# Performance work log

Measured on AMD Instinct MI355X. Metric: run time of the kernel, lower is better.

## Reference

```python
import jax, jax.numpy as jnp
import numpy as np

N = 4096
C = 8192
D = 64
MARGIN = 0.1
ALPHA = 32.0


def setup_inputs() -> dict:
    key = jax.random.key(0)
    k1, k2, k3, k4 = jax.random.split(key, 4)
    embeddings = jax.random.normal(k1, (N, D), dtype=jnp.float32)
    labels = jax.random.randint(k2, (N,), 0, C)
    # kaiming_normal_(mode='fan_out') on a (C, D) tensor -> std = sqrt(2/C)
    mean_proxies = jax.random.normal(k3, (C, D), dtype=jnp.float32) * np.sqrt(2.0 / C)
    log_variance_proxies = jax.random.normal(k4, (C, D), dtype=jnp.float32) * np.sqrt(2.0 / C)
    return {
        "embeddings": embeddings,
        "labels": labels,
        "mean_proxies": mean_proxies,
        "log_variance_proxies": log_variance_proxies,
    }


def _mls_scores(e, mu, logvar):
    """score[i,j] = -0.5 * sum_d[(e_id - mu_jd)^2 * exp(-logvar_jd) + logvar_jd].
    Expanded into GEMMs to avoid materializing the (N, C, D) broadcast tensor."""
    inv_var = jnp.exp(-logvar)                                  # (C, D)
    e2_term = (e * e) @ inv_var.T                               # (N, C)
    cross = e @ (mu * inv_var).T                                # (N, C)
    const = jnp.sum(mu * mu * inv_var + logvar, axis=1)         # (C,)
    return -0.5 * (e2_term - 2.0 * cross + const[None, :])      # (N, C)


def reference(embeddings, labels, mean_proxies, log_variance_proxies):
    score_mat = _mls_scores(embeddings, mean_proxies, log_variance_proxies)  # (N, C)
    pos_mask = jax.nn.one_hot(labels, C, dtype=score_mat.dtype)              # (N, C)

    pos_e = -ALPHA * (score_mat - MARGIN)
    neg_e = ALPHA * (score_mat + MARGIN)
    m = jnp.max(pos_e)  # NOTE: original code uses max(pos_exp) for BOTH terms
    pos_exp = jnp.exp(pos_e - m)
    neg_exp = jnp.exp(neg_e - m)

    counts = jnp.sum(pos_mask, axis=0)                   # (C,)
    num_valid = jnp.sum(counts != 0).astype(score_mat.dtype)

    pos_sim_sum = jnp.sum(jnp.where(pos_mask == 1, pos_exp, 0.0), axis=0)  # (C,)
    neg_sim_sum = jnp.sum(jnp.where(pos_mask == 0, neg_exp, 0.0), axis=0)  # (C,)

    pos_term = jnp.sum(jnp.log1p(pos_sim_sum) + m) / num_valid
    neg_term = jnp.sum(jnp.log1p(neg_sim_sum) + m) / C
    return pos_term + neg_term
```

## Files before the change

kernel.cpp:

```cpp
#include <hip/hip_runtime.h>
#include <hip/hip_bf16.h>
#include <math.h>


#define N_EMB 4096
#define C_CLS 8192
#define D_DIM 64
#define K_DIM 128
#define NCB 4

#define S2_F    23.083120654223414f
#define B2_F     4.616624130844683f
#define NEGC2_F  9.233248261689366f
#define LN2_F    0.6931471805599453f

typedef __attribute__((ext_vector_type(8))) __bf16 bf16x8;
typedef __attribute__((ext_vector_type(4))) __bf16 bf16x4;
typedef __attribute__((ext_vector_type(16))) float f32x16;
typedef __attribute__((ext_vector_type(4))) int i32x4;

__device__ __forceinline__ void async_ld16(void* lds, const void* g) {
  __builtin_amdgcn_global_load_lds(
      (__attribute__((address_space(1))) void*)g,
      (__attribute__((address_space(3))) void*)lds, 16, 0, 0);
}

__device__ __forceinline__ float fexp2(float x) {
  float r;
  asm("v_exp_f32 %0, %1" : "=v"(r) : "v"(x));
  return r;
}

__global__ void k_prep(const float* __restrict__ emb,
                       const float* __restrict__ mp,
                       const float* __restrict__ lvp,
                       __bf16* __restrict__ wsA,
                       __bf16* __restrict__ wsB,
                       float* __restrict__ constv) {
  const int wave = (int)((blockIdx.x * blockDim.x + threadIdx.x) >> 6);
  const int lane = threadIdx.x & 63;
  const int sub = lane >> 4, q = lane & 15;
  const int row = wave * 4 + sub;
  if (row < N_EMB) {
    float4 e4 = *(const float4*)&emb[row * D_DIM + q * 4];
    bf16x4 sq = {(__bf16)(e4.x * e4.x), (__bf16)(e4.y * e4.y),
                 (__bf16)(e4.z * e4.z), (__bf16)(e4.w * e4.w)};
    bf16x4 ev = {(__bf16)e4.x, (__bf16)e4.y, (__bf16)e4.z, (__bf16)e4.w};
    *(bf16x4*)&wsA[row * K_DIM + q * 4] = sq;
    *(bf16x4*)&wsA[row * K_DIM + D_DIM + q * 4] = ev;
  } else {
    const int j = row - N_EMB;
    float4 mu4 = *(const float4*)&mp[j * D_DIM + q * 4];
    float4 lv4 = *(const float4*)&lvp[j * D_DIM + q * 4];
    float iv0 = __expf(-lv4.x), iv1 = __expf(-lv4.y);
    float iv2 = __expf(-lv4.z), iv3 = __expf(-lv4.w);
    bf16x4 ivv = {(__bf16)iv0, (__bf16)iv1, (__bf16)iv2, (__bf16)iv3};
    bf16x4 mv = {(__bf16)(-2.0f * mu4.x * iv0), (__bf16)(-2.0f * mu4.y * iv1),
                 (__bf16)(-2.0f * mu4.z * iv2), (__bf16)(-2.0f * mu4.w * iv3)};
    *(bf16x4*)&wsB[j * K_DIM + q * 4] = ivv;
    *(bf16x4*)&wsB[j * K_DIM + D_DIM + q * 4] = mv;
    float t = fmaf(mu4.x * mu4.x, iv0, lv4.x)
            + fmaf(mu4.y * mu4.y, iv1, lv4.y)
            + fmaf(mu4.z * mu4.z, iv2, lv4.z)
            + fmaf(mu4.w * mu4.w, iv3, lv4.w);
    #pragma unroll
    for (int s = 8; s >= 1; s >>= 1) t += __shfl_xor(t, s);
    if (q == 0) constv[j] = t;
  }
}

__global__ __launch_bounds__(256, 2) void k_main(
    const __bf16* __restrict__ wsA, const __bf16* __restrict__ wsB,
    const float* __restrict__ constv, const int* __restrict__ labels,
    float* __restrict__ wsM, float* __restrict__ wsP, float* __restrict__ wsN) {
  __shared__ __align__(16) char As[32768];
  __shared__ __align__(16) char Bs[32768];
  __shared__ float colred[2][128][3];

  const int tid = threadIdx.x;
  const int rb  = blockIdx.x & 31;
  const int cbg = blockIdx.x >> 5;

  const char* Ag = (const char*)(wsA + (size_t)rb * 128 * K_DIM);
  const char* Bgb = (const char*)(wsB + (size_t)(cbg * NCB) * 128 * K_DIM);
  #pragma unroll
  for (int it = 0; it < 8; ++it) {
    int L = it * 256 + tid;
    int r = L >> 4, cs = L & 15;
    int goff = r * 256 + ((cs ^ (r & 15)) << 4);
    async_ld16(As + L * 16, Ag + goff);
  }
  #pragma unroll
  for (int it = 0; it < 8; ++it) {
    int L = it * 256 + tid;
    int r = L >> 4, cs = L & 15;
    int goff = r * 256 + ((cs ^ (r & 15)) << 4);
    async_ld16(Bs + L * 16, Bgb + goff);
  }

  const int wv = tid >> 6, lane = tid & 63;
  const int wr = wv >> 1, wc = wv & 1;
  const int l31 = lane & 31, kg = lane >> 5;
  const int l15 = lane & 15;

  i32x4 labv[2][4];
  #pragma unroll
  for (int mi = 0; mi < 2; ++mi)
    #pragma unroll
    for (int g = 0; g < 4; ++g)
      labv[mi][g] = *(const i32x4*)&labels[rb * 128 + wr * 64 + mi * 32 +
                                           4 * kg + 8 * g];
  float cvv[NCB][2];
  #pragma unroll
  for (int cbi = 0; cbi < NCB; ++cbi)
    #pragma unroll
    for (int ni = 0; ni < 2; ++ni)
      cvv[cbi][ni] = constv[(cbg * NCB + cbi) * 128 + wc * 64 + ni * 32 + l31];

  __syncthreads();

  #pragma unroll
  for (int cbi = 0; cbi < NCB; ++cbi) {
    const int cb = cbg * NCB + cbi;

    f32x16 acc[2][2];
    #pragma unroll
    for (int mi = 0; mi < 2; ++mi)
      #pragma unroll
      for (int ni = 0; ni < 2; ++ni)
        #pragma unroll
        for (int r = 0; r < 16; ++r) acc[mi][ni][r] = 0.f;

    #pragma unroll
    for (int kk = 0; kk < 8; ++kk) {
      const int c = kk * 2 + kg;
      const int cofs = (c ^ l15) << 4;
      bf16x8 af[2], bfr[2];
      #pragma unroll
      for (int mi = 0; mi < 2; ++mi)
        af[mi] = *(const bf16x8*)(As + (wr * 64 + mi * 32 + l31) * 256 + cofs);
      #pragma unroll
      for (int ni = 0; ni < 2; ++ni)
        bfr[ni] = *(const bf16x8*)(Bs + (wc * 64 + ni * 32 + l31) * 256 + cofs);
      #pragma unroll
      for (int mi = 0; mi < 2; ++mi)
        #pragma unroll
        for (int ni = 0; ni < 2; ++ni)
          acc[mi][ni] = __builtin_amdgcn_mfma_f32_32x32x16_bf16(
              af[mi], bfr[ni], acc[mi][ni], 0, 0, 0);
    }

    __syncthreads();

    if (cbi + 1 < NCB) {
      const char* Bg = Bgb + (size_t)(cbi + 1) * 32768;
      #pragma unroll
      for (int it = 0; it < 8; ++it) {
        int L = it * 256 + tid;
        int r = L >> 4, cs = L & 15;
        int goff = r * 256 + ((cs ^ (r & 15)) << 4);
        async_ld16(Bs + L * 16, Bg + goff);
      }
    }

    #pragma unroll
    for (int ni = 0; ni < 2; ++ni) {
      const int col_local = wc * 64 + ni * 32 + l31;
      const int gcol = cb * 128 + col_local;
      const float pcv = fmaf(S2_F, cvv[cbi][ni], B2_F);
      float lmax = -1e30f;
      #pragma unroll
      for (int mi = 0; mi < 2; ++mi)
        #pragma unroll
        for (int r = 0; r < 16; ++r) {
          float pe = fmaf(S2_F, acc[mi][ni][r], pcv);
          acc[mi][ni][r] = pe;
          lmax = fmaxf(lmax, pe);
        }
      lmax = fmaxf(lmax, __shfl_xor(lmax, 32));
      const float negb = NEGC2_F - lmax;
      float ps = 0.f, ns = 0.f;
      #pragma unroll
      for (int mi = 0; mi < 2; ++mi)
        #pragma unroll
        for (int r = 0; r < 16; ++r) {
          float pe = acc[mi][ni][r];
          float ex = fexp2(negb - pe);
          ns += ex;
          if (labv[mi][r >> 2][r & 3] == gcol) {
            ns -= ex;
            ps += fexp2(pe - lmax);
          }
        }
      ps += __shfl_xor(ps, 32);
      ns += __shfl_xor(ns, 32);
      if (kg == 0) {
        colred[wr][col_local][0] = lmax;
        colred[wr][col_local][1] = ps;
        colred[wr][col_local][2] = ns;
      }
    }
    __syncthreads();
    if (tid < 128) {
      float m0 = colred[0][tid][0], m1 = colred[1][tid][0];
      float M = fmaxf(m0, m1);
      float s0 = fexp2(m0 - M), s1 = fexp2(m1 - M);
      int gcol = cb * 128 + tid;
      wsM[rb * C_CLS + gcol] = M;
      wsP[rb * C_CLS + gcol] = fmaf(colred[0][tid][1], s0, colred[1][tid][1] * s1);
      wsN[rb * C_CLS + gcol] = fmaf(colred[0][tid][2], s0, colred[1][tid][2] * s1);
    }
  }
}

__global__ __launch_bounds__(256) void k_red1(
    const float* __restrict__ wsM, const float* __restrict__ wsP,
    const float* __restrict__ wsN, const int* __restrict__ labels,
    float* __restrict__ Mcol, float* __restrict__ Pcol,
    float* __restrict__ Ncol, int* __restrict__ nvp) {
  __shared__ float red[8][32][3];
  __shared__ int fl[32];
  const int tid = threadIdx.x;
  const int col = tid & 31, part = tid >> 5;
  const int bx = blockIdx.x;
  const int j = bx * 32 + col;

  if (tid < 32) fl[tid] = 0;

  float m4[4];
  float M = -1e30f;
  #pragma unroll
  for (int r = 0; r < 4; ++r) {
    m4[r] = wsM[(part * 4 + r) * C_CLS + j];
    M = fmaxf(M, m4[r]);
  }
  float ps = 0.f, ns = 0.f;
  #pragma unroll
  for (int r = 0; r < 4; ++r) {
    float s = fexp2(m4[r] - M);
    ps = fmaf(wsP[(part * 4 + r) * C_CLS + j], s, ps);
    ns = fmaf(wsN[(part * 4 + r) * C_CLS + j], s, ns);
  }
  red[part][col][0] = M; red[part][col][1] = ps; red[part][col][2] = ns;
  __syncthreads();

  #pragma unroll
  for (int it = 0; it < 4; ++it) {
    int4 lb = ((const int4*)labels)[it * 256 + tid];
    if ((lb.x >> 5) == bx) fl[lb.x & 31] = 1;
    if ((lb.y >> 5) == bx) fl[lb.y & 31] = 1;
    if ((lb.z >> 5) == bx) fl[lb.z & 31] = 1;
    if ((lb.w >> 5) == bx) fl[lb.w & 31] = 1;
  }

  if (part == 0) {
    float Mx = -1e30f;
    #pragma unroll
    for (int p = 0; p < 8; ++p) Mx = fmaxf(Mx, red[p][col][0]);
    float P = 0.f, Nn = 0.f;
    #pragma unroll
    for (int p = 0; p < 8; ++p) {
      float s = fexp2(red[p][col][0] - Mx);
      P = fmaf(red[p][col][1], s, P);
      Nn = fmaf(red[p][col][2], s, Nn);
    }
    Mcol[j] = Mx; Pcol[j] = P; Ncol[j] = Nn;
  }
  __syncthreads();
  if (tid < 64) {
    int f = (tid < 32) ? fl[tid] : 0;
    #pragma unroll
    for (int s = 32; s >= 1; s >>= 1) f += __shfl_xor(f, s);
    if (tid == 0) nvp[bx] = f;
  }
}

__global__ __launch_bounds__(1024) void k_fin(
    const float* __restrict__ Mcol, const float* __restrict__ Pcol,
    const float* __restrict__ Ncol, const int* __restrict__ nvp,
    float* __restrict__ out) {
  __shared__ float sA[16], sB[16];
  __shared__ int sI[16];
  const int tid = threadIdx.x;
  const int wv = tid >> 6, lane = tid & 63;

  float colMv[8], colPv[8], colNv[8];
  #pragma unroll
  for (int k = 0; k < 8; ++k) {
    int i = k * 1024 + tid;
    colMv[k] = Mcol[i]; colPv[k] = Pcol[i]; colNv[k] = Ncol[i];
  }
  int nv = (tid < 256) ? nvp[tid] : 0;

  float gm = -1e30f;
  #pragma unroll
  for (int k = 0; k < 8; ++k) gm = fmaxf(gm, colMv[k]);
  #pragma unroll
  for (int s = 32; s >= 1; s >>= 1) {
    gm = fmaxf(gm, __shfl_xor(gm, s));
    nv += __shfl_xor(nv, s);
  }
  if (lane == 0) { sA[wv] = gm; sI[wv] = nv; }
  __syncthreads();
  if (tid == 0) {
    float mm = -1e30f; int n = 0;
    #pragma unroll
    for (int k = 0; k < 16; ++k) { mm = fmaxf(mm, sA[k]); n += sI[k]; }
    sA[0] = mm; sI[0] = n;
  }
  __syncthreads();
  const float m = sA[0];
  const int num_valid = sI[0];
  __syncthreads();
  float pt = 0.f, nt = 0.f;
  #pragma unroll
  for (int k = 0; k < 8; ++k) {
    float s = fexp2(colMv[k] - m);
    pt += log1pf(colPv[k] * s);
    nt += log1pf(colNv[k] * s);
  }
  #pragma unroll
  for (int s = 32; s >= 1; s >>= 1) {
    pt += __shfl_xor(pt, s);
    nt += __shfl_xor(nt, s);
  }
  if (lane == 0) { sA[wv] = pt; sB[wv] = nt; }
  __syncthreads();
  if (tid == 0) {
    float sp = 0.f, sn = 0.f;
    #pragma unroll
    for (int k = 0; k < 16; ++k) { sp += sA[k]; sn += sB[k]; }
    const float mn = m * LN2_F;
    out[0] = (sp + (float)C_CLS * mn) / (float)num_valid
           + (sn + (float)C_CLS * mn) / (float)C_CLS;
  }
}

extern "C" void kernel_launch(void* const* d_in, const int* in_sizes, int n_in,
                              void* d_out, int out_size, void* d_ws, size_t ws_size,
                              hipStream_t stream) {
  const float* emb    = (const float*)d_in[0];
  const int*   labels = (const int*)d_in[1];
  const float* mp     = (const float*)d_in[2];
  const float* lvp    = (const float*)d_in[3];
  float* out = (float*)d_out;

  char* ws = (char*)d_ws;
  __bf16* wsA   = (__bf16*)ws;
  __bf16* wsB   = (__bf16*)(ws + (1u << 20));
  float* constv = (float*)(ws + 3u * (1u << 20));
  float* wsM    = (float*)(ws + 3u * (1u << 20) + (1u << 15));
  float* wsP    = wsM + 32 * C_CLS;
  float* wsN    = wsP + 32 * C_CLS;
  float* Mcol   = wsN + 32 * C_CLS;
  float* Pcol   = Mcol + C_CLS;
  float* Ncol   = Pcol + C_CLS;
  int*   nvp    = (int*)(Ncol + C_CLS);

  hipLaunchKernelGGL(k_prep, dim3(768), dim3(256), 0, stream,
                     emb, mp, lvp, wsA, wsB, constv);
  hipLaunchKernelGGL(k_main, dim3(32 * (C_CLS / 128 / NCB)), dim3(256), 0, stream,
                     wsA, wsB, constv, labels, wsM, wsP, wsN);
  hipLaunchKernelGGL(k_red1, dim3(256), dim3(256), 0, stream,
                     wsM, wsP, wsN, labels, Mcol, Pcol, Ncol, nvp);
  hipLaunchKernelGGL(k_fin, dim3(1), dim3(1024), 0, stream,
                     Mcol, Pcol, Ncol, nvp, out);
}
```

Measured before the change: 98.82 us.

## Fuse final reduction into red kernel via last-block ticket; streamline epilogue max/exp

Merges the single-block final kernel into the column-reduction kernel with an atomic ticket counter, so the last finishing block computes the scalar loss and one kernel launch goes away. The counter is reset in the prep kernel. In the main GEMM epilogue, the score scaling is folded into the exp arguments, the max uses v_max3 trees on the raw accumulators, and the negative sum is split across two accumulators to shorten dependency chains. The log1p for tiny values is replaced by its identity approximation. This adds a threadfence/atomic and heavy register use (96 floats) in the last block.

```diff
diff --git a/kernel.cpp b/kernel.cpp
--- a/kernel.cpp
+++ b/kernel.cpp
@@ -31,12 +31,20 @@
   return r;
 }
 
+__device__ __forceinline__ float fmax3(float a, float b, float c) {
+  float r;
+  asm("v_max3_f32 %0, %1, %2, %3" : "=v"(r) : "v"(a), "v"(b), "v"(c));
+  return r;
+}
+
 __global__ void k_prep(const float* __restrict__ emb,
                        const float* __restrict__ mp,
                        const float* __restrict__ lvp,
                        __bf16* __restrict__ wsA,
                        __bf16* __restrict__ wsB,
-                       float* __restrict__ constv) {
+                       float* __restrict__ constv,
+                       int* __restrict__ counter) {
+  if (blockIdx.x == 0 && threadIdx.x == 0) *counter = 0;
   const int wave = (int)((blockIdx.x * blockDim.x + threadIdx.x) >> 6);
   const int lane = threadIdx.x & 63;
   const int sub = lane >> 4, q = lane & 15;
@@ -168,30 +176,45 @@
       const int col_local = wc * 64 + ni * 32 + l31;
       const int gcol = cb * 128 + col_local;
       const float pcv = fmaf(S2_F, cvv[cbi][ni], B2_F);
-      float lmax = -1e30f;
+
+      #define AV(k) acc[(k) >> 4][ni][(k) & 15]
+      float t0 = fmax3(AV(0), AV(1), AV(2));
+      float t1 = fmax3(AV(3), AV(4), AV(5));
+      float t2 = fmax3(AV(6), AV(7), AV(8));
+      float t3 = fmax3(AV(9), AV(10), AV(11));
+      float t4 = fmax3(AV(12), AV(13), AV(14));
+      float t5 = fmax3(AV(15), AV(16), AV(17));
+      float t6 = fmax3(AV(18), AV(19), AV(20));
+      float t7 = fmax3(AV(21), AV(22), AV(23));
+      float t8 = fmax3(AV(24), AV(25), AV(26));
+      float t9 = fmax3(AV(27), AV(28), AV(29));
+      float ta = fmaxf(AV(30), AV(31));
+      #undef AV
+      float u0 = fmax3(t0, t1, t2);
+      float u1 = fmax3(t3, t4, t5);
+      float u2 = fmax3(t6, t7, t8);
+      float u3 = fmax3(t9, ta, u0);
+      float rm = fmax3(u1, u2, u3);
+      rm = fmaxf(rm, __shfl_xor(rm, 32));
+
+      const float pm = S2_F * rm;
+      const float lmax = pm + pcv;
+      const float cn = NEGC2_F - pm - 2.0f * pcv;
+
+      float nsa = 0.f, nsb = 0.f, ps = 0.f;
       #pragma unroll
       for (int mi = 0; mi < 2; ++mi)
         #pragma unroll
         for (int r = 0; r < 16; ++r) {
-          float pe = fmaf(S2_F, acc[mi][ni][r], pcv);
-          acc[mi][ni][r] = pe;
-          lmax = fmaxf(lmax, pe);
-        }
-      lmax = fmaxf(lmax, __shfl_xor(lmax, 32));
-      const float negb = NEGC2_F - lmax;
-      float ps = 0.f, ns = 0.f;
-      #pragma unroll
-      for (int mi = 0; mi < 2; ++mi)
-        #pragma unroll
-        for (int r = 0; r < 16; ++r) {
-          float pe = acc[mi][ni][r];
-          float ex = fexp2(negb - pe);
-          ns += ex;
+          float a = acc[mi][ni][r];
+          float ex = fexp2(fmaf(-S2_F, a, cn));
+          if (r & 1) nsb += ex; else nsa += ex;
           if (labv[mi][r >> 2][r & 3] == gcol) {
-            ns -= ex;
-            ps += fexp2(pe - lmax);
+            if (r & 1) nsb -= ex; else nsa -= ex;
+            ps += fexp2(fmaf(S2_F, a, -pm));
           }
         }
+      float ns = nsa + nsb;
       ps += __shfl_xor(ps, 32);
       ns += __shfl_xor(ns, 32);
       if (kg == 0) {
@@ -213,13 +236,15 @@
   }
 }
 
-__global__ __launch_bounds__(256) void k_red1(
+__global__ __launch_bounds__(256) void k_red(
     const float* __restrict__ wsM, const float* __restrict__ wsP,
     const float* __restrict__ wsN, const int* __restrict__ labels,
     float* __restrict__ Mcol, float* __restrict__ Pcol,
-    float* __restrict__ Ncol, int* __restrict__ nvp) {
+    float* __restrict__ Ncol, int* __restrict__ nvp,
+    int* __restrict__ counter, float* __restrict__ out) {
   __shared__ float red[8][32][3];
   __shared__ int fl[32];
+  __shared__ int ticket;
   const int tid = threadIdx.x;
   const int col = tid & 31, part = tid >> 5;
   const int bx = blockIdx.x;
@@ -273,40 +298,37 @@
     for (int s = 32; s >= 1; s >>= 1) f += __shfl_xor(f, s);
     if (tid == 0) nvp[bx] = f;
   }
-}
-
-__global__ __launch_bounds__(1024) void k_fin(
-    const float* __restrict__ Mcol, const float* __restrict__ Pcol,
-    const float* __restrict__ Ncol, const int* __restrict__ nvp,
-    float* __restrict__ out) {
-  __shared__ float sA[16], sB[16];
-  __shared__ int sI[16];
-  const int tid = threadIdx.x;
-  const int wv = tid >> 6, lane = tid & 63;
-
-  float colMv[8], colPv[8], colNv[8];
-  #pragma unroll
-  for (int k = 0; k < 8; ++k) {
-    int i = k * 1024 + tid;
-    colMv[k] = Mcol[i]; colPv[k] = Pcol[i]; colNv[k] = Ncol[i];
-  }
-  int nv = (tid < 256) ? nvp[tid] : 0;
-
+
+  __threadfence();
+  __syncthreads();
+  if (tid == 0) ticket = atomicAdd(counter, 1);
+  __syncthreads();
+  if (ticket != 255) return;
+  __threadfence();
+
+  __shared__ float sA[4], sB[4];
+  __shared__ int sI[4];
+  const int wvf = tid >> 6, lane = tid & 63;
+
+  float Mv[32], Pv[32], Nv[32];
   float gm = -1e30f;
   #pragma unroll
-  for (int k = 0; k < 8; ++k) gm = fmaxf(gm, colMv[k]);
+  for (int k = 0; k < 32; ++k) {
+    int i = k * 256 + tid;
+    Mv[k] = Mcol[i]; Pv[k] = Pcol[i]; Nv[k] = Ncol[i];
+    gm = fmaxf(gm, Mv[k]);
+  }
+  int nv = nvp[tid];
   #pragma unroll
   for (int s = 32; s >= 1; s >>= 1) {
     gm = fmaxf(gm, __shfl_xor(gm, s));
     nv += __shfl_xor(nv, s);
   }
-  if (lane == 0) { sA[wv] = gm; sI[wv] = nv; }
+  if (lane == 0) { sA[wvf] = gm; sI[wvf] = nv; }
   __syncthreads();
   if (tid == 0) {
-    float mm = -1e30f; int n = 0;
-    #pragma unroll
-    for (int k = 0; k < 16; ++k) { mm = fmaxf(mm, sA[k]); n += sI[k]; }
-    sA[0] = mm; sI[0] = n;
+    float mm = fmaxf(fmaxf(sA[0], sA[1]), fmaxf(sA[2], sA[3]));
+    sA[0] = mm; sI[0] = sI[0] + sI[1] + sI[2] + sI[3];
   }
   __syncthreads();
   const float m = sA[0];
@@ -314,22 +336,23 @@
   __syncthreads();
   float pt = 0.f, nt = 0.f;
   #pragma unroll
-  for (int k = 0; k < 8; ++k) {
-    float s = fexp2(colMv[k] - m);
-    pt += log1pf(colPv[k] * s);
-    nt += log1pf(colNv[k] * s);
+  for (int k = 0; k < 32; ++k) {
+    float s = fexp2(Mv[k] - m);
+    float xp = Pv[k] * s;
+    float xn = Nv[k] * s;
+    pt += (xp > 1e-7f) ? log1pf(xp) : xp;
+    nt += (xn > 1e-7f) ? log1pf(xn) : xn;
   }
   #pragma unroll
   for (int s = 32; s >= 1; s >>= 1) {
     pt += __shfl_xor(pt, s);
     nt += __shfl_xor(nt, s);
   }
-  if (lane == 0) { sA[wv] = pt; sB[wv] = nt; }
+  if (lane == 0) { sA[wvf] = pt; sB[wvf] = nt; }
   __syncthreads();
   if (tid == 0) {
-    float sp = 0.f, sn = 0.f;
-    #pragma unroll
-    for (int k = 0; k < 16; ++k) { sp += sA[k]; sn += sB[k]; }
+    float sp = sA[0] + sA[1] + sA[2] + sA[3];
+    float sn = sB[0] + sB[1] + sB[2] + sB[3];
     const float mn = m * LN2_F;
     out[0] = (sp + (float)C_CLS * mn) / (float)num_valid
            + (sn + (float)C_CLS * mn) / (float)C_CLS;
@@ -356,13 +379,12 @@
   float* Pcol   = Mcol + C_CLS;
   float* Ncol   = Pcol + C_CLS;
   int*   nvp    = (int*)(Ncol + C_CLS);
+  int*   counter = nvp + 256;
 
   hipLaunchKernelGGL(k_prep, dim3(768), dim3(256), 0, stream,
-                     emb, mp, lvp, wsA, wsB, constv);
+                     emb, mp, lvp, wsA, wsB, constv, counter);
   hipLaunchKernelGGL(k_main, dim3(32 * (C_CLS / 128 / NCB)), dim3(256), 0, stream,
                      wsA, wsB, constv, labels, wsM, wsP, wsN);
-  hipLaunchKernelGGL(k_red1, dim3(256), dim3(256), 0, stream,
-                     wsM, wsP, wsN, labels, Mcol, Pcol, Ncol, nvp);
-  hipLaunchKernelGGL(k_fin, dim3(1), dim3(1024), 0, stream,
-                     Mcol, Pcol, Ncol, nvp, out);
-}
+  hipLaunchKernelGGL(k_red, dim3(256), dim3(256), 0, stream,
+                     wsM, wsP, wsN, labels, Mcol, Pcol, Ncol, nvp, counter, out);
+}
```

Result: slower. 114.6 us (+15.9%).
